# Kernel optimization log

Measured on AMD Instinct MI355X. Metric: run time of the kernel, lower is better.

Reference implementation:

```python
import jax, jax.numpy as jnp
import numpy as np

HEADS, DIM_HEAD, C, B, HS, WS = 8, 64, 512, 2, 48, 48


def setup_inputs() -> dict:
    key = jax.random.key(0)
    ks = jax.random.split(key, 9)
    s = 0.02
    return {
        "hidden_states": jax.random.normal(ks[0], (B, C, HS, WS), jnp.float32),
        "Wq": jax.random.normal(ks[1], (HEADS, DIM_HEAD, C), jnp.float32) * s,
        "bq": jax.random.normal(ks[2], (HEADS, DIM_HEAD), jnp.float32) * s,
        "Wk": jax.random.normal(ks[3], (HEADS, DIM_HEAD, C), jnp.float32) * s,
        "bk": jax.random.normal(ks[4], (HEADS, DIM_HEAD), jnp.float32) * s,
        "Wv": jax.random.normal(ks[5], (HEADS, DIM_HEAD, C), jnp.float32) * s,
        "bv": jax.random.normal(ks[6], (HEADS, DIM_HEAD), jnp.float32) * s,
        "Wo": jax.random.normal(ks[7], (C, HEADS * DIM_HEAD), jnp.float32) * s,
        "bo": jax.random.normal(ks[8], (C,), jnp.float32) * s,
    }


def reference(hidden_states, Wq, bq, Wk, bk, Wv, bv, Wo, bo):
    # hidden_states: [B, C, H, W]; per-head 1x1 convs == per-head linear over C.
    b, c, h, w = hidden_states.shape
    hw = h * w
    x = hidden_states.reshape(b, c, hw)  # [B, C, HW]
    # Batched per-head projections (fuses the per-head Conv2d loop).
    q = jnp.einsum('bcs,ndc->bnsd', x, Wq) + bq[None, :, None, :]  # [B, n, HW, d]
    k = jnp.einsum('bcs,ndc->bnsd', x, Wk) + bk[None, :, None, :]
    v = jnp.einsum('bcs,ndc->bnsd', x, Wv) + bv[None, :, None, :]
    scale = 1.0 / jnp.sqrt(jnp.asarray(DIM_HEAD, hidden_states.dtype))
    scores = jnp.einsum('bnqd,bnkd->bnqk', q, k) * scale  # [B, n, HW, HW]
    probs = jax.nn.softmax(scores, axis=-1)
    attn = jnp.einsum('bnqk,bnkd->bnqd', probs, v)  # [B, n, HW, d]
    # concat heads along last dim (matches torch.cat(..., dim=-1))
    attn = attn.transpose(0, 2, 1, 3).reshape(b, hw, HEADS * DIM_HEAD)
    out = attn @ Wo.T + bo  # [B, HW, C] (to_out[0]; to_out[1] dropout = identity)
    out = out.reshape(b, h, w, c).transpose(0, 3, 1, 2)  # [B, C, H, W]
    return out
```

## Files before the change

kernel.cpp:

```cpp
#include <hip/hip_runtime.h>
#include <hip/hip_bf16.h>

#define HEADS 8
#define DHEAD 64
#define CDIM  512
#define SEQ   2304
#define ND    512

typedef unsigned short u16;
typedef unsigned int   u32;
typedef __attribute__((ext_vector_type(8))) short short8;
typedef __attribute__((ext_vector_type(4))) float f32x4;

#define QSCALE 0.18033688011112043f

__device__ __forceinline__ u16 f2bf(float f) {
    union { float f; u32 u; } x; x.f = f;
    u32 r = x.u + 0x7FFFu + ((x.u >> 16) & 1u);
    return (u16)(r >> 16);
}
__device__ __forceinline__ float bf2f(u16 v) {
    union { u32 u; float f; } x; x.u = ((u32)v) << 16; return x.f;
}
__device__ __forceinline__ u32 pkbf(float a, float b) {
    union { float f; u32 u; } x, y; x.f = a; y.f = b;
    return __builtin_amdgcn_perm(y.u + 0x8000u, x.u + 0x8000u, 0x07060302u);
}
__device__ __forceinline__ f32x4 mfma16(short8 a, short8 b, f32x4 c) {
    return __builtin_amdgcn_mfma_f32_16x16x32_bf16(a, b, c, 0, 0, 0);
}
__device__ __forceinline__ void cp16(const void* g, void* l) {
    __builtin_amdgcn_global_load_lds(
        (const __attribute__((address_space(1))) u32*)(uintptr_t)g,
        (__attribute__((address_space(3))) u32*)(u32)(uintptr_t)l,
        16, 0, 0);
}
__device__ __forceinline__ int kperm_inv(int r) {
    return (r & ~0x1C) | ((r & 0x0C) << 1) | ((r & 0x10) >> 2);
}

__global__ void prep_kernel(const float* __restrict__ H,
                            const float* __restrict__ Wq, const float* __restrict__ Wk,
                            const float* __restrict__ Wv, const float* __restrict__ Wo,
                            u16* __restrict__ Wqkv, u16* __restrict__ Wob,
                            u16* __restrict__ X) {
    __shared__ float tile[32][33];
    const int t = threadIdx.x;
    const int bx = blockIdx.x;
    if (bx < 4096) {
        int idx = bx * 256 + t;
        const int N1 = CDIM * ND;
        if (idx < N1)             Wqkv[idx] = f2bf(Wq[idx]);
        else if (idx < 2 * N1)    Wqkv[idx] = f2bf(Wk[idx - N1]);
        else if (idx < 3 * N1)    Wqkv[idx] = f2bf(Wv[idx - 2 * N1]);
        else                      Wob[idx - 3 * N1] = f2bf(Wo[idx - 3 * N1]);
    } else {
        int bb = bx - 4096;
        int st = bb % 72, ct = (bb / 72) % 16, b = bb / (72 * 16);
        int tx = t & 31, ty = t >> 5;
#pragma unroll
        for (int k = 0; k < 4; ++k) {
            int c = ct * 32 + ty + k * 8;
            tile[ty + k * 8][tx] = H[((size_t)b * CDIM + c) * SEQ + st * 32 + tx];
        }
        __syncthreads();
#pragma unroll
        for (int k = 0; k < 4; ++k) {
            int s = st * 32 + ty + k * 8;
            X[((size_t)b * SEQ + s) * CDIM + ct * 32 + tx] = f2bf(tile[tx][ty + k * 8]);
        }
    }
}

__global__ __launch_bounds__(256) void gemm_qkv_kernel(
        const u16* __restrict__ W, const u16* __restrict__ X,
        const float* __restrict__ bq, const float* __restrict__ bk, const float* __restrict__ bv,
        u16* __restrict__ Q, u16* __restrict__ K, u16* __restrict__ V) {
    __shared__ __align__(16) u16 sm[2 * (64 * 64 + 128 * 64)];
    const int n0 = blockIdx.x * 128;
    const int m0 = blockIdx.y * 64;
    const int b  = blockIdx.z;
    const int t = threadIdx.x;
    const int lane = t & 63, w = t >> 6;
    const int l16 = lane & 15, quad = lane >> 4;
    const int x7 = l16 & 7;
    const int srow = t >> 3, scol = (t & 7) * 8;
    const int scol_sw = ((t & 7) ^ (srow & 7)) * 8;
    const u16* Xb = X + (size_t)b * SEQ * CDIM;

    f32x4 acc[4][2] = {};

    {
        u16* As = sm; u16* Bs = sm + 64 * 64;
#pragma unroll
        for (int it = 0; it < 2; ++it) {
            int r2 = it * 32 + srow;
            cp16(&W[(size_t)(m0 + r2) * 512 + scol_sw], &As[r2 * 64 + scol]);
        }
#pragma unroll
        for (int it = 0; it < 4; ++it) {
            int r2 = it * 32 + srow;
            cp16(&Xb[(size_t)(n0 + r2) * 512 + scol_sw], &Bs[r2 * 64 + scol]);
        }
    }
    for (int kb = 0; kb < 512; kb += 64) {
        const int pb = (kb >> 6) & 1;
        u16* As = sm + pb * 12288;
        u16* Bs = As + 64 * 64;
        __syncthreads();
        if (kb + 64 < 512) {
            u16* An = sm + (pb ^ 1) * 12288;
            u16* Bn = An + 64 * 64;
#pragma unroll
            for (int it = 0; it < 2; ++it) {
                int r2 = it * 32 + srow;
                cp16(&W[(size_t)(m0 + r2) * 512 + kb + 64 + scol_sw], &An[r2 * 64 + scol]);
            }
#pragma unroll
            for (int it = 0; it < 4; ++it) {
                int r2 = it * 32 + srow;
                cp16(&Xb[(size_t)(n0 + r2) * 512 + kb + 64 + scol_sw], &Bn[r2 * 64 + scol]);
            }
        }
#pragma unroll
        for (int kk = 0; kk < 2; ++kk) {
            const int co = ((kk * 4 + quad) ^ x7) * 8;
            short8 af[4], bfr[2];
#pragma unroll
            for (int i = 0; i < 4; ++i)
                af[i] = *(const short8*)&As[(i * 16 + l16) * 64 + co];
#pragma unroll
            for (int j = 0; j < 2; ++j)
                bfr[j] = *(const short8*)&Bs[(w * 32 + j * 16 + l16) * 64 + co];
#pragma unroll
            for (int i = 0; i < 4; ++i)
#pragma unroll
                for (int j = 0; j < 2; ++j)
                    acc[i][j] = mfma16(af[i], bfr[j], acc[i][j]);
        }
    }

    if (m0 < 1024) {
        const bool isQ = (m0 < 512);
        const float* bias = isQ ? bq : bk;
        const float sc = isQ ? QSCALE : 1.0f;
        const int mq = isQ ? m0 : m0 - 512;
        u16* dst = isQ ? Q : K;
#pragma unroll
        for (int j = 0; j < 2; ++j) {
            int s = n0 + w * 32 + j * 16 + l16;
#pragma unroll
            for (int i = 0; i < 4; ++i) {
                int mm = mq + i * 16 + quad * 4;
                uint2 val;
                val.x = pkbf((acc[i][j][0] + bias[mm + 0]) * sc, (acc[i][j][1] + bias[mm + 1]) * sc);
                val.y = pkbf((acc[i][j][2] + bias[mm + 2]) * sc, (acc[i][j][3] + bias[mm + 3]) * sc);
                *(uint2*)&dst[(((size_t)(b * 8 + (mm >> 6))) * SEQ + s) * 64 + (mm & 63)] = val;
            }
        }
    } else {
#pragma unroll
        for (int j = 0; j < 2; ++j) {
            int s = n0 + w * 32 + j * 16 + l16;
#pragma unroll
            for (int i = 0; i < 4; ++i) {
                int mbase = m0 - 1024 + i * 16 + quad * 4;
#pragma unroll
                for (int r = 0; r < 4; ++r) {
                    int mm = mbase + r;
                    V[((size_t)(b * 512 + mm)) * SEQ + s] = f2bf(acc[i][j][r] + bv[mm]);
                }
            }
        }
    }
}

__global__ __launch_bounds__(256, 3) void attn_partial(
        const u16* __restrict__ Q,
        const u16* __restrict__ K,
        const u16* __restrict__ Vt,
        u16* __restrict__ Opart,
        float* __restrict__ Lpart) {
    __shared__ __align__(16) u16 sm[2 * 8192];
    const int pair = blockIdx.x & 15, qt = blockIdx.x >> 4;
    const int c = blockIdx.y;
    const int b = pair >> 3, h = pair & 7;
    const int t = threadIdx.x, lane = t & 63, w = t >> 6;
    const int l16 = lane & 15, quad = lane >> 4;
    const int x7 = l16 & 7;
    const int srow = t >> 3;
    const int scol = (t & 7) * 8;
    const int scol_sw = ((t & 7) ^ (srow & 7)) * 8;
    const int kinv0 = kperm_inv(srow), kinv1 = kperm_inv(32 + srow);
    const int cA = (quad ^ x7) * 8;
    const int cB = (quad ^ x7 ^ 4) * 8;

    const u16* Qg = Q + ((size_t)pair * SEQ + qt * 192) * 64;
    const int rA = w * 16 + l16;
    short8 qf[3][2];
#pragma unroll
    for (int G = 0; G < 3; ++G) {
        qf[G][0] = *(const short8*)&Qg[(size_t)(G * 64 + rA) * 64 + quad * 8];
        qf[G][1] = *(const short8*)&Qg[(size_t)(G * 64 + rA) * 64 + 32 + quad * 8];
    }

    const u16* Kg = K  + ((size_t)pair * SEQ + c * 576) * 64;
    const u16* Vg = Vt + ((size_t)(b * 512 + h * 64)) * SEQ + c * 576;

    float lacc[3] = {0.f, 0.f, 0.f};
    f32x4 o[3][4] = {};

    {
        u16* Ks = sm; u16* Vs = sm + 4096;
        cp16(&Kg[(size_t)kinv0 * 64 + scol_sw], &Ks[srow * 64 + scol]);
        cp16(&Kg[(size_t)kinv1 * 64 + scol_sw], &Ks[(32 + srow) * 64 + scol]);
        cp16(&Vg[(size_t)srow * SEQ + scol_sw],        &Vs[srow * 64 + scol]);
        cp16(&Vg[(size_t)(32 + srow) * SEQ + scol_sw], &Vs[(32 + srow) * 64 + scol]);
    }
    for (int kt = 0; kt < 9; ++kt) {
        const int pb = kt & 1;
        const u16* Ks = sm + pb * 8192;
        const u16* Vs = Ks + 4096;
        __syncthreads();
        if (kt < 8) {
            u16* Kn = sm + (pb ^ 1) * 8192;
            u16* Vn = Kn + 4096;
            cp16(&Kg[(size_t)((kt + 1) * 64 + kinv0) * 64 + scol_sw], &Kn[srow * 64 + scol]);
            cp16(&Kg[(size_t)((kt + 1) * 64 + kinv1) * 64 + scol_sw], &Kn[(32 + srow) * 64 + scol]);
            cp16(&Vg[(size_t)srow * SEQ + (kt + 1) * 64 + scol_sw],        &Vn[srow * 64 + scol]);
            cp16(&Vg[(size_t)(32 + srow) * SEQ + (kt + 1) * 64 + scol_sw], &Vn[(32 + srow) * 64 + scol]);
        }
        f32x4 sacc[3][4];
#pragma unroll
        for (int j = 0; j < 4; ++j) {
            short8 kf0 = *(const short8*)&Ks[(j * 16 + l16) * 64 + cA];
            short8 kf1 = *(const short8*)&Ks[(j * 16 + l16) * 64 + cB];
#pragma unroll
            for (int G = 0; G < 3; ++G) {
                f32x4 z = {0.f, 0.f, 0.f, 0.f};
                z = mfma16(kf0, qf[G][0], z);
                sacc[G][j] = mfma16(kf1, qf[G][1], z);
            }
        }
        u32 pk[3][8];
#pragma unroll
        for (int G = 0; G < 3; ++G)
#pragma unroll
            for (int j = 0; j < 4; ++j) {
                float e0 = __builtin_amdgcn_exp2f(sacc[G][j][0]);
                float e1 = __builtin_amdgcn_exp2f(sacc[G][j][1]);
                float e2 = __builtin_amdgcn_exp2f(sacc[G][j][2]);
                float e3 = __builtin_amdgcn_exp2f(sacc[G][j][3]);
                lacc[G] += (e0 + e1) + (e2 + e3);
                pk[G][2 * j]     = pkbf(e0, e1);
                pk[G][2 * j + 1] = pkbf(e2, e3);
            }
#pragma unroll
        for (int g = 0; g < 2; ++g) {
            const int cg = g ? cB : cA;
#pragma unroll
            for (int i = 0; i < 4; ++i) {
                short8 vf = *(const short8*)&Vs[(i * 16 + l16) * 64 + cg];
#pragma unroll
                for (int G = 0; G < 3; ++G) {
                    short8 pf;
                    u32* pw = (u32*)&pf;
                    pw[0] = pk[G][4 * g + 0];
                    pw[1] = pk[G][4 * g + 1];
                    pw[2] = pk[G][4 * g + 2];
                    pw[3] = pk[G][4 * g + 3];
                    o[G][i] = mfma16(vf, pf, o[G][i]);
                }
            }
        }
    }
    float linv[3];
#pragma unroll
    for (int G = 0; G < 3; ++G) {
        float lr = lacc[G];
        lr += __shfl_xor(lr, 16);
        lr += __shfl_xor(lr, 32);
        if (quad == 0) Lpart[((size_t)(c * 16 + pair)) * SEQ + qt * 192 + G * 64 + rA] = lr;
        linv[G] = 1.0f / lr;
    }
    const size_t orow = ((size_t)(c * 16 + pair)) * SEQ + qt * 192;

    __syncthreads();
#pragma unroll
    for (int G = 0; G < 3; ++G)
#pragma unroll
        for (int i = 0; i < 4; ++i) {
            uint2 pkv;
            pkv.x = pkbf(o[G][i][0] * linv[G], o[G][i][1] * linv[G]);
            pkv.y = pkbf(o[G][i][2] * linv[G], o[G][i][3] * linv[G]);
            *(uint2*)&sm[(G * 64 + rA) * 72 + i * 16 + quad * 4] = pkv;
        }
    __syncthreads();
#pragma unroll
    for (int it = 0; it < 6; ++it) {
        int v = it * 256 + t;
        int row = v >> 3, col = (v & 7) * 8;
        *(uint4*)&Opart[(orow + row) * 64 + col] = *(const uint4*)&sm[row * 72 + col];
    }
}

__global__ __launch_bounds__(256) void attn_combine(
        const u16* __restrict__ Opart, const float* __restrict__ Lpart,
        u16* __restrict__ At) {
    const int bid = blockIdx.x;
    const int pair = bid / 144, sb = bid % 144;
    const int tid = threadIdx.x;
    const int rl = tid >> 4, dg = tid & 15;
    const int s = sb * 16 + rl;
    const int b = pair >> 3, h = pair & 7;
    float wc[4], L = 0.f;
#pragma unroll
    for (int c = 0; c < 4; ++c) {
        wc[c] = Lpart[(size_t)(c * 16 + pair) * SEQ + s];
        L += wc[c];
    }
    float invL = 1.0f / L;
    float acc[4] = {0.f, 0.f, 0.f, 0.f};
#pragma unroll
    for (int c = 0; c < 4; ++c) {
        ushort4 v = *(const ushort4*)&Opart[((size_t)(c * 16 + pair) * SEQ + s) * 64 + dg * 4];
        acc[0] += wc[c] * bf2f(v.x);
        acc[1] += wc[c] * bf2f(v.y);
        acc[2] += wc[c] * bf2f(v.z);
        acc[3] += wc[c] * bf2f(v.w);
    }
    uint2 outv;
    outv.x = pkbf(acc[0] * invL, acc[1] * invL);
    outv.y = pkbf(acc[2] * invL, acc[3] * invL);
    *(uint2*)&At[((size_t)b * SEQ + s) * ND + h * 64 + dg * 4] = outv;
}

__global__ __launch_bounds__(256) void gemm_out_kernel(
        const u16* __restrict__ Wob, const u16* __restrict__ At,
        const float* __restrict__ bo, float* __restrict__ out) {
    __shared__ __align__(16) u16 sm[2 * 8192];
    const int n0 = blockIdx.x * 64;
    const int m0 = blockIdx.y * 64;
    const int b  = blockIdx.z;
    const int t = threadIdx.x;
    const int lane = t & 63, w = t >> 6;
    const int l16 = lane & 15, quad = lane >> 4;
    const int x7 = l16 & 7;
    const int srow = t >> 3, scol = (t & 7) * 8;
    const int scol_sw = ((t & 7) ^ (srow & 7)) * 8;
    const u16* Ab = At + (size_t)b * SEQ * ND;

    f32x4 acc[4] = {};

    {
        u16* As = sm; u16* Bs = sm + 4096;
#pragma unroll
        for (int it = 0; it < 2; ++it) {
            int r2 = it * 32 + srow;
            cp16(&Wob[(size_t)(m0 + r2) * 512 + scol_sw], &As[r2 * 64 + scol]);
            cp16(&Ab [(size_t)(n0 + r2) * 512 + scol_sw], &Bs[r2 * 64 + scol]);
        }
    }
    for (int kb = 0; kb < 512; kb += 64) {
        const int pb = (kb >> 6) & 1;
        const u16* As = sm + pb * 8192;
        const u16* Bs = As + 4096;
        __syncthreads();
        if (kb + 64 < 512) {
            u16* An = sm + (pb ^ 1) * 8192;
            u16* Bn = An + 4096;
#pragma unroll
            for (int it = 0; it < 2; ++it) {
                int r2 = it * 32 + srow;
                cp16(&Wob[(size_t)(m0 + r2) * 512 + kb + 64 + scol_sw], &An[r2 * 64 + scol]);
                cp16(&Ab [(size_t)(n0 + r2) * 512 + kb + 64 + scol_sw], &Bn[r2 * 64 + scol]);
            }
        }
#pragma unroll
        for (int kk = 0; kk < 2; ++kk) {
            const int co = ((kk * 4 + quad) ^ x7) * 8;
            short8 af[4];
#pragma unroll
            for (int i = 0; i < 4; ++i)
                af[i] = *(const short8*)&As[(i * 16 + l16) * 64 + co];
            short8 bfr = *(const short8*)&Bs[(w * 16 + l16) * 64 + co];
#pragma unroll
            for (int i = 0; i < 4; ++i)
                acc[i] = mfma16(af[i], bfr, acc[i]);
        }
    }
#pragma unroll
    for (int i = 0; i < 4; ++i) {
        int cbase = m0 + i * 16 + quad * 4;
        int s = n0 + w * 16 + l16;
#pragma unroll
        for (int r = 0; r < 4; ++r) {
            int cc = cbase + r;
            out[((size_t)(b * 512 + cc)) * SEQ + s] = acc[i][r] + bo[cc];
        }
    }
}

extern "C" void kernel_launch(void* const* d_in, const int* in_sizes, int n_in,
                              void* d_out, int out_size, void* d_ws, size_t ws_size,
                              hipStream_t stream) {
    const float* H  = (const float*)d_in[0];
    const float* Wq = (const float*)d_in[1];
    const float* bq = (const float*)d_in[2];
    const float* Wk = (const float*)d_in[3];
    const float* bk = (const float*)d_in[4];
    const float* Wv = (const float*)d_in[5];
    const float* bv = (const float*)d_in[6];
    const float* Wo = (const float*)d_in[7];
    const float* bo = (const float*)d_in[8];
    float* out = (float*)d_out;

    u16* ws    = (u16*)d_ws;
    u16* Wqkv  = ws;
    u16* Wob   = Wqkv  + 1536 * 512;
    u16* Xbf   = Wob   + 512 * 512;
    u16* Qb    = Xbf   + 2 * SEQ * CDIM;
    u16* Kb    = Qb    + 2 * SEQ * ND;
    u16* Vb    = Kb    + 2 * SEQ * ND;
    u16* At    = Vb    + 2 * SEQ * ND;
    u16* Opart = At    + 2 * SEQ * ND;
    float* Lpart = (float*)(Opart + 4 * 16 * SEQ * 64);

    prep_kernel<<<6400, 256, 0, stream>>>(H, Wq, Wk, Wv, Wo, Wqkv, Wob, Xbf);
    gemm_qkv_kernel<<<dim3(18, 24, 2), 256, 0, stream>>>(Wqkv, Xbf, bq, bk, bv, Qb, Kb, Vb);
    attn_partial<<<dim3(192, 4), 256, 0, stream>>>(Qb, Kb, Vb, Opart, Lpart);
    attn_combine<<<2304, 256, 0, stream>>>(Opart, Lpart, At);
    gemm_out_kernel<<<dim3(36, 8, 2), 256, 0, stream>>>(Wob, At, bo, out);
}
```

Before: 135.0 us.

## Fuse all stages into one persistent cooperative kernel with grid syncs

Replaces the five separate launches (prep, QKV GEMM, attention partial, combine, output GEMM) with a single persistent cooperative kernel. Blocks loop over each stage's work items and separate the stages with grid-wide syncs. This removes per-launch overhead and inter-kernel gaps. In exchange it adds grid barrier costs, caps the grid at occupancy×256 blocks, and gives every stage the shared-memory footprint and register bounds of the largest one.

```diff
diff --git a/kernel.cpp b/kernel.cpp
--- a/kernel.cpp
+++ b/kernel.cpp
@@ -1,5 +1,8 @@
 #include <hip/hip_runtime.h>
 #include <hip/hip_bf16.h>
+#include <hip/hip_cooperative_groups.h>
+
+namespace cg = cooperative_groups;
 
 #define HEADS 8
 #define DHEAD 64
@@ -39,364 +42,359 @@
     return (r & ~0x1C) | ((r & 0x0C) << 1) | ((r & 0x10) >> 2);
 }
 
-__global__ void prep_kernel(const float* __restrict__ H,
-                            const float* __restrict__ Wq, const float* __restrict__ Wk,
-                            const float* __restrict__ Wv, const float* __restrict__ Wo,
-                            u16* __restrict__ Wqkv, u16* __restrict__ Wob,
-                            u16* __restrict__ X) {
-    __shared__ float tile[32][33];
+__global__ __launch_bounds__(256, 3) void mega_kernel(
+        const float* __restrict__ H,
+        const float* __restrict__ Wq, const float* __restrict__ bq,
+        const float* __restrict__ Wk, const float* __restrict__ bk,
+        const float* __restrict__ Wv, const float* __restrict__ bv,
+        const float* __restrict__ Wo, const float* __restrict__ bo,
+        float* __restrict__ out, u16* __restrict__ ws) {
+    u16* Wqkv  = ws;
+    u16* Wob   = Wqkv  + 1536 * 512;
+    u16* Xbf   = Wob   + 512 * 512;
+    u16* Qb    = Xbf   + 2 * SEQ * CDIM;
+    u16* Kb    = Qb    + 2 * SEQ * ND;
+    u16* Vb    = Kb    + 2 * SEQ * ND;
+    u16* At    = Vb    + 2 * SEQ * ND;
+    u16* Opart = At    + 2 * SEQ * ND;
+    float* Lpart = (float*)(Opart + 64 * SEQ * 64);
+
+    __shared__ __align__(16) u16 sm[24576];
+
+    cg::grid_group gg = cg::this_grid();
     const int t = threadIdx.x;
-    const int bx = blockIdx.x;
-    if (bx < 4096) {
-        int idx = bx * 256 + t;
-        const int N1 = CDIM * ND;
-        if (idx < N1)             Wqkv[idx] = f2bf(Wq[idx]);
-        else if (idx < 2 * N1)    Wqkv[idx] = f2bf(Wk[idx - N1]);
-        else if (idx < 3 * N1)    Wqkv[idx] = f2bf(Wv[idx - 2 * N1]);
-        else                      Wob[idx - 3 * N1] = f2bf(Wo[idx - 3 * N1]);
-    } else {
-        int bb = bx - 4096;
-        int st = bb % 72, ct = (bb / 72) % 16, b = bb / (72 * 16);
-        int tx = t & 31, ty = t >> 5;
-#pragma unroll
-        for (int k = 0; k < 4; ++k) {
-            int c = ct * 32 + ty + k * 8;
-            tile[ty + k * 8][tx] = H[((size_t)b * CDIM + c) * SEQ + st * 32 + tx];
-        }
-        __syncthreads();
-#pragma unroll
-        for (int k = 0; k < 4; ++k) {
-            int s = st * 32 + ty + k * 8;
-            X[((size_t)b * SEQ + s) * CDIM + ct * 32 + tx] = f2bf(tile[tx][ty + k * 8]);
-        }
-    }
-}
-
-__global__ __launch_bounds__(256) void gemm_qkv_kernel(
-        const u16* __restrict__ W, const u16* __restrict__ X,
-        const float* __restrict__ bq, const float* __restrict__ bk, const float* __restrict__ bv,
-        u16* __restrict__ Q, u16* __restrict__ K, u16* __restrict__ V) {
-    __shared__ __align__(16) u16 sm[2 * (64 * 64 + 128 * 64)];
-    const int n0 = blockIdx.x * 128;
-    const int m0 = blockIdx.y * 64;
-    const int b  = blockIdx.z;
-    const int t = threadIdx.x;
+    const int bid = blockIdx.x, nb = gridDim.x;
     const int lane = t & 63, w = t >> 6;
-    const int l16 = lane & 15, quad = lane >> 4;
-    const int x7 = l16 & 7;
-    const int srow = t >> 3, scol = (t & 7) * 8;
-    const int scol_sw = ((t & 7) ^ (srow & 7)) * 8;
-    const u16* Xb = X + (size_t)b * SEQ * CDIM;
-
-    f32x4 acc[4][2] = {};
-
-    {
-        u16* As = sm; u16* Bs = sm + 64 * 64;
-#pragma unroll
-        for (int it = 0; it < 2; ++it) {
-            int r2 = it * 32 + srow;
-            cp16(&W[(size_t)(m0 + r2) * 512 + scol_sw], &As[r2 * 64 + scol]);
-        }
-#pragma unroll
-        for (int it = 0; it < 4; ++it) {
-            int r2 = it * 32 + srow;
-            cp16(&Xb[(size_t)(n0 + r2) * 512 + scol_sw], &Bs[r2 * 64 + scol]);
-        }
-    }
-    for (int kb = 0; kb < 512; kb += 64) {
-        const int pb = (kb >> 6) & 1;
-        u16* As = sm + pb * 12288;
-        u16* Bs = As + 64 * 64;
-        __syncthreads();
-        if (kb + 64 < 512) {
-            u16* An = sm + (pb ^ 1) * 12288;
-            u16* Bn = An + 64 * 64;
-#pragma unroll
-            for (int it = 0; it < 2; ++it) {
-                int r2 = it * 32 + srow;
-                cp16(&W[(size_t)(m0 + r2) * 512 + kb + 64 + scol_sw], &An[r2 * 64 + scol]);
-            }
-#pragma unroll
-            for (int it = 0; it < 4; ++it) {
-                int r2 = it * 32 + srow;
-                cp16(&Xb[(size_t)(n0 + r2) * 512 + kb + 64 + scol_sw], &Bn[r2 * 64 + scol]);
-            }
-        }
-#pragma unroll
-        for (int kk = 0; kk < 2; ++kk) {
-            const int co = ((kk * 4 + quad) ^ x7) * 8;
-            short8 af[4], bfr[2];
-#pragma unroll
-            for (int i = 0; i < 4; ++i)
-                af[i] = *(const short8*)&As[(i * 16 + l16) * 64 + co];
-#pragma unroll
-            for (int j = 0; j < 2; ++j)
-                bfr[j] = *(const short8*)&Bs[(w * 32 + j * 16 + l16) * 64 + co];
-#pragma unroll
-            for (int i = 0; i < 4; ++i)
-#pragma unroll
-                for (int j = 0; j < 2; ++j)
-                    acc[i][j] = mfma16(af[i], bfr[j], acc[i][j]);
-        }
-    }
-
-    if (m0 < 1024) {
-        const bool isQ = (m0 < 512);
-        const float* bias = isQ ? bq : bk;
-        const float sc = isQ ? QSCALE : 1.0f;
-        const int mq = isQ ? m0 : m0 - 512;
-        u16* dst = isQ ? Q : K;
-#pragma unroll
-        for (int j = 0; j < 2; ++j) {
-            int s = n0 + w * 32 + j * 16 + l16;
-#pragma unroll
-            for (int i = 0; i < 4; ++i) {
-                int mm = mq + i * 16 + quad * 4;
-                uint2 val;
-                val.x = pkbf((acc[i][j][0] + bias[mm + 0]) * sc, (acc[i][j][1] + bias[mm + 1]) * sc);
-                val.y = pkbf((acc[i][j][2] + bias[mm + 2]) * sc, (acc[i][j][3] + bias[mm + 3]) * sc);
-                *(uint2*)&dst[(((size_t)(b * 8 + (mm >> 6))) * SEQ + s) * 64 + (mm & 63)] = val;
-            }
-        }
-    } else {
-#pragma unroll
-        for (int j = 0; j < 2; ++j) {
-            int s = n0 + w * 32 + j * 16 + l16;
-#pragma unroll
-            for (int i = 0; i < 4; ++i) {
-                int mbase = m0 - 1024 + i * 16 + quad * 4;
-#pragma unroll
-                for (int r = 0; r < 4; ++r) {
-                    int mm = mbase + r;
-                    V[((size_t)(b * 512 + mm)) * SEQ + s] = f2bf(acc[i][j][r] + bv[mm]);
-                }
-            }
-        }
-    }
-}
-
-__global__ __launch_bounds__(256, 3) void attn_partial(
-        const u16* __restrict__ Q,
-        const u16* __restrict__ K,
-        const u16* __restrict__ Vt,
-        u16* __restrict__ Opart,
-        float* __restrict__ Lpart) {
-    __shared__ __align__(16) u16 sm[2 * 8192];
-    const int pair = blockIdx.x & 15, qt = blockIdx.x >> 4;
-    const int c = blockIdx.y;
-    const int b = pair >> 3, h = pair & 7;
-    const int t = threadIdx.x, lane = t & 63, w = t >> 6;
     const int l16 = lane & 15, quad = lane >> 4;
     const int x7 = l16 & 7;
     const int srow = t >> 3;
     const int scol = (t & 7) * 8;
     const int scol_sw = ((t & 7) ^ (srow & 7)) * 8;
-    const int kinv0 = kperm_inv(srow), kinv1 = kperm_inv(32 + srow);
-    const int cA = (quad ^ x7) * 8;
-    const int cB = (quad ^ x7 ^ 4) * 8;
-
-    const u16* Qg = Q + ((size_t)pair * SEQ + qt * 192) * 64;
-    const int rA = w * 16 + l16;
-    short8 qf[3][2];
-#pragma unroll
-    for (int G = 0; G < 3; ++G) {
-        qf[G][0] = *(const short8*)&Qg[(size_t)(G * 64 + rA) * 64 + quad * 8];
-        qf[G][1] = *(const short8*)&Qg[(size_t)(G * 64 + rA) * 64 + 32 + quad * 8];
+
+    {
+        float* tile = (float*)sm;
+        const int tx = t & 31, ty = t >> 5;
+        for (int u = bid; u < 6400; u += nb) {
+            if (u < 4096) {
+                int idx = u * 256 + t;
+                const int N1 = CDIM * ND;
+                if (idx < N1)             Wqkv[idx] = f2bf(Wq[idx]);
+                else if (idx < 2 * N1)    Wqkv[idx] = f2bf(Wk[idx - N1]);
+                else if (idx < 3 * N1)    Wqkv[idx] = f2bf(Wv[idx - 2 * N1]);
+                else                      Wob[idx - 3 * N1] = f2bf(Wo[idx - 3 * N1]);
+            } else {
+                int bb = u - 4096;
+                int st = bb % 72, ct = (bb / 72) % 16, b = bb / (72 * 16);
+#pragma unroll
+                for (int k = 0; k < 4; ++k) {
+                    int c = ct * 32 + ty + k * 8;
+                    tile[(ty + k * 8) * 33 + tx] = H[((size_t)b * CDIM + c) * SEQ + st * 32 + tx];
+                }
+                __syncthreads();
+#pragma unroll
+                for (int k = 0; k < 4; ++k) {
+                    int s = st * 32 + ty + k * 8;
+                    X:
+                    Xbf[((size_t)b * SEQ + s) * CDIM + ct * 32 + tx] = f2bf(tile[tx * 33 + ty + k * 8]);
+                }
+                __syncthreads();
+            }
+        }
     }
-
-    const u16* Kg = K  + ((size_t)pair * SEQ + c * 576) * 64;
-    const u16* Vg = Vt + ((size_t)(b * 512 + h * 64)) * SEQ + c * 576;
-
-    float lacc[3] = {0.f, 0.f, 0.f};
-    f32x4 o[3][4] = {};
-
-    {
-        u16* Ks = sm; u16* Vs = sm + 4096;
-        cp16(&Kg[(size_t)kinv0 * 64 + scol_sw], &Ks[srow * 64 + scol]);
-        cp16(&Kg[(size_t)kinv1 * 64 + scol_sw], &Ks[(32 + srow) * 64 + scol]);
-        cp16(&Vg[(size_t)srow * SEQ + scol_sw],        &Vs[srow * 64 + scol]);
-        cp16(&Vg[(size_t)(32 + srow) * SEQ + scol_sw], &Vs[(32 + srow) * 64 + scol]);
-    }
-    for (int kt = 0; kt < 9; ++kt) {
-        const int pb = kt & 1;
-        const u16* Ks = sm + pb * 8192;
-        const u16* Vs = Ks + 4096;
+    gg.sync();
+
+    for (int u = bid; u < 864; u += nb) {
+        const int n0 = (u % 18) * 128;
+        const int m0 = ((u / 18) % 24) * 64;
+        const int b  = u / 432;
+        const u16* Xb = Xbf + (size_t)b * SEQ * CDIM;
+        f32x4 acc[4][2] = {};
         __syncthreads();
-        if (kt < 8) {
-            u16* Kn = sm + (pb ^ 1) * 8192;
-            u16* Vn = Kn + 4096;
-            cp16(&Kg[(size_t)((kt + 1) * 64 + kinv0) * 64 + scol_sw], &Kn[srow * 64 + scol]);
-            cp16(&Kg[(size_t)((kt + 1) * 64 + kinv1) * 64 + scol_sw], &Kn[(32 + srow) * 64 + scol]);
-            cp16(&Vg[(size_t)srow * SEQ + (kt + 1) * 64 + scol_sw],        &Vn[srow * 64 + scol]);
-            cp16(&Vg[(size_t)(32 + srow) * SEQ + (kt + 1) * 64 + scol_sw], &Vn[(32 + srow) * 64 + scol]);
-        }
-        f32x4 sacc[3][4];
-#pragma unroll
-        for (int j = 0; j < 4; ++j) {
-            short8 kf0 = *(const short8*)&Ks[(j * 16 + l16) * 64 + cA];
-            short8 kf1 = *(const short8*)&Ks[(j * 16 + l16) * 64 + cB];
-#pragma unroll
-            for (int G = 0; G < 3; ++G) {
-                f32x4 z = {0.f, 0.f, 0.f, 0.f};
-                z = mfma16(kf0, qf[G][0], z);
-                sacc[G][j] = mfma16(kf1, qf[G][1], z);
-            }
-        }
-        u32 pk[3][8];
-#pragma unroll
-        for (int G = 0; G < 3; ++G)
-#pragma unroll
-            for (int j = 0; j < 4; ++j) {
-                float e0 = __builtin_amdgcn_exp2f(sacc[G][j][0]);
-                float e1 = __builtin_amdgcn_exp2f(sacc[G][j][1]);
-                float e2 = __builtin_amdgcn_exp2f(sacc[G][j][2]);
-                float e3 = __builtin_amdgcn_exp2f(sacc[G][j][3]);
-                lacc[G] += (e0 + e1) + (e2 + e3);
-                pk[G][2 * j]     = pkbf(e0, e1);
-                pk[G][2 * j + 1] = pkbf(e2, e3);
-            }
-#pragma unroll
-        for (int g = 0; g < 2; ++g) {
-            const int cg = g ? cB : cA;
-#pragma unroll
-            for (int i = 0; i < 4; ++i) {
-                short8 vf = *(const short8*)&Vs[(i * 16 + l16) * 64 + cg];
-#pragma unroll
-                for (int G = 0; G < 3; ++G) {
-                    short8 pf;
-                    u32* pw = (u32*)&pf;
-                    pw[0] = pk[G][4 * g + 0];
-                    pw[1] = pk[G][4 * g + 1];
-                    pw[2] = pk[G][4 * g + 2];
-                    pw[3] = pk[G][4 * g + 3];
-                    o[G][i] = mfma16(vf, pf, o[G][i]);
-                }
-            }
-        }
-    }
-    float linv[3];
-#pragma unroll
-    for (int G = 0; G < 3; ++G) {
-        float lr = lacc[G];
-        lr += __shfl_xor(lr, 16);
-        lr += __shfl_xor(lr, 32);
-        if (quad == 0) Lpart[((size_t)(c * 16 + pair)) * SEQ + qt * 192 + G * 64 + rA] = lr;
-        linv[G] = 1.0f / lr;
-    }
-    const size_t orow = ((size_t)(c * 16 + pair)) * SEQ + qt * 192;
-
-    __syncthreads();
-#pragma unroll
-    for (int G = 0; G < 3; ++G)
-#pragma unroll
-        for (int i = 0; i < 4; ++i) {
-            uint2 pkv;
-            pkv.x = pkbf(o[G][i][0] * linv[G], o[G][i][1] * linv[G]);
-            pkv.y = pkbf(o[G][i][2] * linv[G], o[G][i][3] * linv[G]);
-            *(uint2*)&sm[(G * 64 + rA) * 72 + i * 16 + quad * 4] = pkv;
-        }
-    __syncthreads();
-#pragma unroll
-    for (int it = 0; it < 6; ++it) {
-        int v = it * 256 + t;
-        int row = v >> 3, col = (v & 7) * 8;
-        *(uint4*)&Opart[(orow + row) * 64 + col] = *(const uint4*)&sm[row * 72 + col];
-    }
-}
-
-__global__ __launch_bounds__(256) void attn_combine(
-        const u16* __restrict__ Opart, const float* __restrict__ Lpart,
-        u16* __restrict__ At) {
-    const int bid = blockIdx.x;
-    const int pair = bid / 144, sb = bid % 144;
-    const int tid = threadIdx.x;
-    const int rl = tid >> 4, dg = tid & 15;
-    const int s = sb * 16 + rl;
-    const int b = pair >> 3, h = pair & 7;
-    float wc[4], L = 0.f;
-#pragma unroll
-    for (int c = 0; c < 4; ++c) {
-        wc[c] = Lpart[(size_t)(c * 16 + pair) * SEQ + s];
-        L += wc[c];
-    }
-    float invL = 1.0f / L;
-    float acc[4] = {0.f, 0.f, 0.f, 0.f};
-#pragma unroll
-    for (int c = 0; c < 4; ++c) {
-        ushort4 v = *(const ushort4*)&Opart[((size_t)(c * 16 + pair) * SEQ + s) * 64 + dg * 4];
-        acc[0] += wc[c] * bf2f(v.x);
-        acc[1] += wc[c] * bf2f(v.y);
-        acc[2] += wc[c] * bf2f(v.z);
-        acc[3] += wc[c] * bf2f(v.w);
-    }
-    uint2 outv;
-    outv.x = pkbf(acc[0] * invL, acc[1] * invL);
-    outv.y = pkbf(acc[2] * invL, acc[3] * invL);
-    *(uint2*)&At[((size_t)b * SEQ + s) * ND + h * 64 + dg * 4] = outv;
-}
-
-__global__ __launch_bounds__(256) void gemm_out_kernel(
-        const u16* __restrict__ Wob, const u16* __restrict__ At,
-        const float* __restrict__ bo, float* __restrict__ out) {
-    __shared__ __align__(16) u16 sm[2 * 8192];
-    const int n0 = blockIdx.x * 64;
-    const int m0 = blockIdx.y * 64;
-    const int b  = blockIdx.z;
-    const int t = threadIdx.x;
-    const int lane = t & 63, w = t >> 6;
-    const int l16 = lane & 15, quad = lane >> 4;
-    const int x7 = l16 & 7;
-    const int srow = t >> 3, scol = (t & 7) * 8;
-    const int scol_sw = ((t & 7) ^ (srow & 7)) * 8;
-    const u16* Ab = At + (size_t)b * SEQ * ND;
-
-    f32x4 acc[4] = {};
-
-    {
-        u16* As = sm; u16* Bs = sm + 4096;
-#pragma unroll
-        for (int it = 0; it < 2; ++it) {
-            int r2 = it * 32 + srow;
-            cp16(&Wob[(size_t)(m0 + r2) * 512 + scol_sw], &As[r2 * 64 + scol]);
-            cp16(&Ab [(size_t)(n0 + r2) * 512 + scol_sw], &Bs[r2 * 64 + scol]);
-        }
-    }
-    for (int kb = 0; kb < 512; kb += 64) {
-        const int pb = (kb >> 6) & 1;
-        const u16* As = sm + pb * 8192;
-        const u16* Bs = As + 4096;
-        __syncthreads();
-        if (kb + 64 < 512) {
-            u16* An = sm + (pb ^ 1) * 8192;
-            u16* Bn = An + 4096;
+        {
+            u16* As = sm; u16* Bs = sm + 4096;
 #pragma unroll
             for (int it = 0; it < 2; ++it) {
                 int r2 = it * 32 + srow;
-                cp16(&Wob[(size_t)(m0 + r2) * 512 + kb + 64 + scol_sw], &An[r2 * 64 + scol]);
-                cp16(&Ab [(size_t)(n0 + r2) * 512 + kb + 64 + scol_sw], &Bn[r2 * 64 + scol]);
-            }
-        }
-#pragma unroll
-        for (int kk = 0; kk < 2; ++kk) {
-            const int co = ((kk * 4 + quad) ^ x7) * 8;
-            short8 af[4];
-#pragma unroll
-            for (int i = 0; i < 4; ++i)
-                af[i] = *(const short8*)&As[(i * 16 + l16) * 64 + co];
-            short8 bfr = *(const short8*)&Bs[(w * 16 + l16) * 64 + co];
-#pragma unroll
-            for (int i = 0; i < 4; ++i)
-                acc[i] = mfma16(af[i], bfr, acc[i]);
+                cp16(&Wqkv[(size_t)(m0 + r2) * 512 + scol_sw], &As[r2 * 64 + scol]);
+            }
+#pragma unroll
+            for (int it = 0; it < 4; ++it) {
+                int r2 = it * 32 + srow;
+                cp16(&Xb[(size_t)(n0 + r2) * 512 + scol_sw], &Bs[r2 * 64 + scol]);
+            }
+        }
+        for (int kb = 0; kb < 512; kb += 64) {
+            const int pb = (kb >> 6) & 1;
+            const u16* As = sm + pb * 12288;
+            const u16* Bs = As + 4096;
+            __syncthreads();
+            if (kb + 64 < 512) {
+                u16* An = sm + (pb ^ 1) * 12288;
+                u16* Bn = An + 4096;
+#pragma unroll
+                for (int it = 0; it < 2; ++it) {
+                    int r2 = it * 32 + srow;
+                    cp16(&Wqkv[(size_t)(m0 + r2) * 512 + kb + 64 + scol_sw], &An[r2 * 64 + scol]);
+                }
+#pragma unroll
+                for (int it = 0; it < 4; ++it) {
+                    int r2 = it * 32 + srow;
+                    cp16(&Xb[(size_t)(n0 + r2) * 512 + kb + 64 + scol_sw], &Bn[r2 * 64 + scol]);
+                }
+            }
+#pragma unroll
+            for (int kk = 0; kk < 2; ++kk) {
+                const int co = ((kk * 4 + quad) ^ x7) * 8;
+                short8 af[4], bfr[2];
+#pragma unroll
+                for (int i = 0; i < 4; ++i)
+                    af[i] = *(const short8*)&As[(i * 16 + l16) * 64 + co];
+#pragma unroll
+                for (int j = 0; j < 2; ++j)
+                    bfr[j] = *(const short8*)&Bs[(w * 32 + j * 16 + l16) * 64 + co];
+#pragma unroll
+                for (int i = 0; i < 4; ++i)
+#pragma unroll
+                    for (int j = 0; j < 2; ++j)
+                        acc[i][j] = mfma16(af[i], bfr[j], acc[i][j]);
+            }
+        }
+        if (m0 < 1024) {
+            const bool isQ = (m0 < 512);
+            const float* bias = isQ ? bq : bk;
+            const float sc = isQ ? QSCALE : 1.0f;
+            const int mq = isQ ? m0 : m0 - 512;
+            u16* dst = isQ ? Qb : Kb;
+#pragma unroll
+            for (int j = 0; j < 2; ++j) {
+                int s = n0 + w * 32 + j * 16 + l16;
+#pragma unroll
+                for (int i = 0; i < 4; ++i) {
+                    int mm = mq + i * 16 + quad * 4;
+                    uint2 val;
+                    val.x = pkbf((acc[i][j][0] + bias[mm + 0]) * sc, (acc[i][j][1] + bias[mm + 1]) * sc);
+                    val.y = pkbf((acc[i][j][2] + bias[mm + 2]) * sc, (acc[i][j][3] + bias[mm + 3]) * sc);
+                    *(uint2*)&dst[(((size_t)(b * 8 + (mm >> 6))) * SEQ + s) * 64 + (mm & 63)] = val;
+                }
+            }
+        } else {
+#pragma unroll
+            for (int j = 0; j < 2; ++j) {
+                int s = n0 + w * 32 + j * 16 + l16;
+#pragma unroll
+                for (int i = 0; i < 4; ++i) {
+                    int mbase = m0 - 1024 + i * 16 + quad * 4;
+#pragma unroll
+                    for (int r = 0; r < 4; ++r) {
+                        int mm = mbase + r;
+                        Vb[((size_t)(b * 512 + mm)) * SEQ + s] = f2bf(acc[i][j][r] + bv[mm]);
+                    }
+                }
+            }
         }
     }
-#pragma unroll
-    for (int i = 0; i < 4; ++i) {
-        int cbase = m0 + i * 16 + quad * 4;
-        int s = n0 + w * 16 + l16;
-#pragma unroll
-        for (int r = 0; r < 4; ++r) {
-            int cc = cbase + r;
-            out[((size_t)(b * 512 + cc)) * SEQ + s] = acc[i][r] + bo[cc];
+    gg.sync();
+
+    {
+        const int kinv0 = kperm_inv(srow), kinv1 = kperm_inv(32 + srow);
+        const int cA = (quad ^ x7) * 8;
+        const int cB = (quad ^ x7 ^ 4) * 8;
+        const int rA = w * 16 + l16;
+        for (int u = bid; u < 768; u += nb) {
+            const int pair = u & 15, qt = (u >> 4) % 12, cc4 = u / 192;
+            const int b = pair >> 3, h = pair & 7;
+            const u16* Qg = Qb + ((size_t)pair * SEQ + qt * 192) * 64;
+            short8 qf[3][2];
+#pragma unroll
+            for (int G = 0; G < 3; ++G) {
+                qf[G][0] = *(const short8*)&Qg[(size_t)(G * 64 + rA) * 64 + quad * 8];
+                qf[G][1] = *(const short8*)&Qg[(size_t)(G * 64 + rA) * 64 + 32 + quad * 8];
+            }
+            const u16* Kg = Kb + ((size_t)pair * SEQ + cc4 * 576) * 64;
+            const u16* Vg = Vb + ((size_t)(b * 512 + h * 64)) * SEQ + cc4 * 576;
+
+            float lacc[3] = {0.f, 0.f, 0.f};
+            f32x4 o[3][4] = {};
+
+            __syncthreads();
+            {
+                u16* Ks = sm; u16* Vs = sm + 4096;
+                cp16(&Kg[(size_t)kinv0 * 64 + scol_sw], &Ks[srow * 64 + scol]);
+                cp16(&Kg[(size_t)kinv1 * 64 + scol_sw], &Ks[(32 + srow) * 64 + scol]);
+                cp16(&Vg[(size_t)srow * SEQ + scol_sw],        &Vs[srow * 64 + scol]);
+                cp16(&Vg[(size_t)(32 + srow) * SEQ + scol_sw], &Vs[(32 + srow) * 64 + scol]);
+            }
+            for (int kt = 0; kt < 9; ++kt) {
+                const int pb = kt & 1;
+                const u16* Ks = sm + pb * 8192;
+                const u16* Vs = Ks + 4096;
+                __syncthreads();
+                if (kt < 8) {
+                    u16* Kn = sm + (pb ^ 1) * 8192;
+                    u16* Vn = Kn + 4096;
+                    cp16(&Kg[(size_t)((kt + 1) * 64 + kinv0) * 64 + scol_sw], &Kn[srow * 64 + scol]);
+                    cp16(&Kg[(size_t)((kt + 1) * 64 + kinv1) * 64 + scol_sw], &Kn[(32 + srow) * 64 + scol]);
+                    cp16(&Vg[(size_t)srow * SEQ + (kt + 1) * 64 + scol_sw],        &Vn[srow * 64 + scol]);
+                    cp16(&Vg[(size_t)(32 + srow) * SEQ + (kt + 1) * 64 + scol_sw], &Vn[(32 + srow) * 64 + scol]);
+                }
+                f32x4 sacc[3][4];
+#pragma unroll
+                for (int j = 0; j < 4; ++j) {
+                    short8 kf0 = *(const short8*)&Ks[(j * 16 + l16) * 64 + cA];
+                    short8 kf1 = *(const short8*)&Ks[(j * 16 + l16) * 64 + cB];
+#pragma unroll
+                    for (int G = 0; G < 3; ++G) {
+                        f32x4 z = {0.f, 0.f, 0.f, 0.f};
+                        z = mfma16(kf0, qf[G][0], z);
+                        sacc[G][j] = mfma16(kf1, qf[G][1], z);
+                    }
+                }
+                u32 pk[3][8];
+#pragma unroll
+                for (int G = 0; G < 3; ++G)
+#pragma unroll
+                    for (int j = 0; j < 4; ++j) {
+                        float e0 = __builtin_amdgcn_exp2f(sacc[G][j][0]);
+                        float e1 = __builtin_amdgcn_exp2f(sacc[G][j][1]);
+                        float e2 = __builtin_amdgcn_exp2f(sacc[G][j][2]);
+                        float e3 = __builtin_amdgcn_exp2f(sacc[G][j][3]);
+                        lacc[G] += (e0 + e1) + (e2 + e3);
+                        pk[G][2 * j]     = pkbf(e0, e1);
+                        pk[G][2 * j + 1] = pkbf(e2, e3);
+                    }
+#pragma unroll
+                for (int g = 0; g < 2; ++g) {
+                    const int cg = g ? cB : cA;
+#pragma unroll
+                    for (int i = 0; i < 4; ++i) {
+                        short8 vf = *(const short8*)&Vs[(i * 16 + l16) * 64 + cg];
+#pragma unroll
+                        for (int G = 0; G < 3; ++G) {
+                            short8 pf;
+                            u32* pw = (u32*)&pf;
+                            pw[0] = pk[G][4 * g + 0];
+                            pw[1] = pk[G][4 * g + 1];
+                            pw[2] = pk[G][4 * g + 2];
+                            pw[3] = pk[G][4 * g + 3];
+                            o[G][i] = mfma16(vf, pf, o[G][i]);
+                        }
+                    }
+                }
+            }
+            float linv[3];
+#pragma unroll
+            for (int G = 0; G < 3; ++G) {
+                float lr = lacc[G];
+                lr += __shfl_xor(lr, 16);
+                lr += __shfl_xor(lr, 32);
+                if (quad == 0) Lpart[((size_t)(cc4 * 16 + pair)) * SEQ + qt * 192 + G * 64 + rA] = lr;
+                linv[G] = 1.0f / lr;
+            }
+            const size_t orow = ((size_t)(cc4 * 16 + pair)) * SEQ + qt * 192;
+            __syncthreads();
+#pragma unroll
+            for (int G = 0; G < 3; ++G)
+#pragma unroll
+                for (int i = 0; i < 4; ++i) {
+                    uint2 pkv;
+                    pkv.x = pkbf(o[G][i][0] * linv[G], o[G][i][1] * linv[G]);
+                    pkv.y = pkbf(o[G][i][2] * linv[G], o[G][i][3] * linv[G]);
+                    *(uint2*)&sm[(G * 64 + rA) * 72 + i * 16 + quad * 4] = pkv;
+                }
+            __syncthreads();
+#pragma unroll
+            for (int it = 0; it < 6; ++it) {
+                int v = it * 256 + t;
+                int row = v >> 3, col = (v & 7) * 8;
+                *(uint4*)&Opart[(orow + row) * 64 + col] = *(const uint4*)&sm[row * 72 + col];
+            }
+        }
+    }
+    gg.sync();
+
+    {
+        const int rl = t >> 4, dg = t & 15;
+        for (int u = bid; u < 2304; u += nb) {
+            const int pair = u / 144, sb = u % 144;
+            const int s = sb * 16 + rl;
+            const int b = pair >> 3, h = pair & 7;
+            float wc[4], L = 0.f;
+#pragma unroll
+            for (int c = 0; c < 4; ++c) {
+                wc[c] = Lpart[(size_t)(c * 16 + pair) * SEQ + s];
+                L += wc[c];
+            }
+            float invL = 1.0f / L;
+            float acc[4] = {0.f, 0.f, 0.f, 0.f};
+#pragma unroll
+            for (int c = 0; c < 4; ++c) {
+                ushort4 v = *(const ushort4*)&Opart[((size_t)(c * 16 + pair) * SEQ + s) * 64 + dg * 4];
+                acc[0] += wc[c] * bf2f(v.x);
+                acc[1] += wc[c] * bf2f(v.y);
+                acc[2] += wc[c] * bf2f(v.z);
+                acc[3] += wc[c] * bf2f(v.w);
+            }
+            uint2 outv;
+            outv.x = pkbf(acc[0] * invL, acc[1] * invL);
+            outv.y = pkbf(acc[2] * invL, acc[3] * invL);
+            *(uint2*)&At[((size_t)b * SEQ + s) * ND + h * 64 + dg * 4] = outv;
+        }
+    }
+    gg.sync();
+
+    for (int u = bid; u < 576; u += nb) {
+        const int n0 = (u % 36) * 64;
+        const int m0 = ((u / 36) % 8) * 64;
+        const int b  = u / 288;
+        const u16* Ab = At + (size_t)b * SEQ * ND;
+        f32x4 acc[4] = {};
+        __syncthreads();
+        {
+            u16* As = sm; u16* Bs = sm + 4096;
+#pragma unroll
+            for (int it = 0; it < 2; ++it) {
+                int r2 = it * 32 + srow;
+                cp16(&Wob[(size_t)(m0 + r2) * 512 + scol_sw], &As[r2 * 64 + scol]);
+                cp16(&Ab [(size_t)(n0 + r2) * 512 + scol_sw], &Bs[r2 * 64 + scol]);
+            }
+        }
+        for (int kb = 0; kb < 512; kb += 64) {
+            const int pb = (kb >> 6) & 1;
+            const u16* As = sm + pb * 8192;
+            const u16* Bs = As + 4096;
+            __syncthreads();
+            if (kb + 64 < 512) {
+                u16* An = sm + (pb ^ 1) * 8192;
+                u16* Bn = An + 4096;
+#pragma unroll
+                for (int it = 0; it < 2; ++it) {
+                    int r2 = it * 32 + srow;
+                    cp16(&Wob[(size_t)(m0 + r2) * 512 + kb + 64 + scol_sw], &An[r2 * 64 + scol]);
+                    cp16(&Ab [(size_t)(n0 + r2) * 512 + kb + 64 + scol_sw], &Bn[r2 * 64 + scol]);
+                }
+            }
+#pragma unroll
+            for (int kk = 0; kk < 2; ++kk) {
+                const int co = ((kk * 4 + quad) ^ x7) * 8;
+                short8 af[4];
+#pragma unroll
+                for (int i = 0; i < 4; ++i)
+                    af[i] = *(const short8*)&As[(i * 16 + l16) * 64 + co];
+                short8 bfr = *(const short8*)&Bs[(w * 16 + l16) * 64 + co];
+#pragma unroll
+                for (int i = 0; i < 4; ++i)
+                    acc[i] = mfma16(af[i], bfr, acc[i]);
+            }
+        }
+#pragma unroll
+        for (int i = 0; i < 4; ++i) {
+            int cbase = m0 + i * 16 + quad * 4;
+            int s = n0 + w * 16 + l16;
+#pragma unroll
+            for (int r = 0; r < 4; ++r) {
+                int cc = cbase + r;
+                out[((size_t)(b * 512 + cc)) * SEQ + s] = acc[i][r] + bo[cc];
+            }
         }
     }
 }
@@ -414,21 +412,16 @@
     const float* Wo = (const float*)d_in[7];
     const float* bo = (const float*)d_in[8];
     float* out = (float*)d_out;
-
-    u16* ws    = (u16*)d_ws;
-    u16* Wqkv  = ws;
-    u16* Wob   = Wqkv  + 1536 * 512;
-    u16* Xbf   = Wob   + 512 * 512;
-    u16* Qb    = Xbf   + 2 * SEQ * CDIM;
-    u16* Kb    = Qb    + 2 * SEQ * ND;
-    u16* Vb    = Kb    + 2 * SEQ * ND;
-    u16* At    = Vb    + 2 * SEQ * ND;
-    u16* Opart = At    + 2 * SEQ * ND;
-    float* Lpart = (float*)(Opart + 4 * 16 * SEQ * 64);
-
-    prep_kernel<<<6400, 256, 0, stream>>>(H, Wq, Wk, Wv, Wo, Wqkv, Wob, Xbf);
-    gemm_qkv_kernel<<<dim3(18, 24, 2), 256, 0, stream>>>(Wqkv, Xbf, bq, bk, bv, Qb, Kb, Vb);
-    attn_partial<<<dim3(192, 4), 256, 0, stream>>>(Qb, Kb, Vb, Opart, Lpart);
-    attn_combine<<<2304, 256, 0, stream>>>(Opart, Lpart, At);
-    gemm_out_kernel<<<dim3(36, 8, 2), 256, 0, stream>>>(Wob, At, bo, out);
-}
+    u16* wsp = (u16*)d_ws;
+
+    int nb = 0;
+    hipError_t e = hipOccupancyMaxActiveBlocksPerMultiprocessor(&nb, mega_kernel, 256, 0);
+    if (e != hipSuccess || nb <= 0) nb = 2;
+    if (nb > 3) nb = 3;
+    dim3 grid(nb * 256);
+
+    void* args[] = {(void*)&H, (void*)&Wq, (void*)&bq, (void*)&Wk, (void*)&bk,
+                    (void*)&Wv, (void*)&bv, (void*)&Wo, (void*)&bo,
+                    (void*)&out, (void*)&wsp};
+    hipLaunchCooperativeKernel((const void*)mega_kernel, grid, dim3(256), args, 0, stream);
+}
```

After: 319.3 us. +136.5%, slower.
